# Optimization experiments

Hardware: AMD Instinct MI355X
Metric: run time of the kernel (lower is better)

## Reference

```python
import jax, jax.numpy as jnp
import numpy as np

EMBED_DIM = 1024
NUM_HEADS = 16
HEAD_DIM = EMBED_DIM // NUM_HEADS
ROPE_BASE = 10000.0


def _rope_angles(seq_len, head_dim):
    inv_freq = 1.0 / (ROPE_BASE ** (jnp.arange(0, head_dim, 2, dtype=jnp.float32) / head_dim))  # [D/2]
    pos = jnp.arange(seq_len, dtype=jnp.float32)
    ang = pos[:, None] * inv_freq[None, :]  # [S, D/2]
    return jnp.cos(ang), jnp.sin(ang)


def _apply_rope(t, cos, sin):
    # t: [B, H, S, D]; rotate-half convention
    d2 = t.shape[-1] // 2
    t1, t2 = t[..., :d2], t[..., d2:]
    return jnp.concatenate([t1 * cos - t2 * sin, t2 * cos + t1 * sin], axis=-1)


def setup_inputs() -> dict:
    key = jax.random.key(0)
    ks = jax.random.split(key, 6)
    B, S, E = 1, 4096, EMBED_DIM
    x = jax.random.normal(ks[0], (B, S, E), dtype=jnp.float32)
    # causal mask: True means masked-out (upper triangle above diagonal)
    mask = jnp.triu(jnp.ones((S, S), dtype=bool), k=1)[None, None, :, :]
    scale = 0.02
    wqkv_w = jax.random.normal(ks[1], (E, 3 * E), dtype=jnp.float32) * scale
    wqkv_b = jax.random.normal(ks[2], (3 * E,), dtype=jnp.float32) * scale
    out_w = jax.random.normal(ks[3], (E, E), dtype=jnp.float32) * scale
    out_b = jax.random.normal(ks[4], (E,), dtype=jnp.float32) * scale
    return {"x": x, "mask": mask, "wqkv_w": wqkv_w, "wqkv_b": wqkv_b, "out_w": out_w, "out_b": out_b}


def reference(x, mask, wqkv_w, wqkv_b, out_w, out_b):
    B, S, E = x.shape
    H, D = NUM_HEADS, HEAD_DIM
    qkv = x @ wqkv_w + wqkv_b  # [B, S, 3E]
    q, k, v = jnp.split(qkv, 3, axis=-1)
    # [B, S, E] -> [B, H, S, D]
    q = q.reshape(B, S, H, D).transpose(0, 2, 1, 3)
    k = k.reshape(B, S, H, D).transpose(0, 2, 1, 3)
    v = v.reshape(B, S, H, D).transpose(0, 2, 1, 3)
    cos, sin = _rope_angles(S, D)  # [S, D/2]
    q = _apply_rope(q, cos, sin)
    k = _apply_rope(k, cos, sin)
    scores = jnp.einsum('bhqd,bhkd->bhqk', q, k) * (D ** -0.5)  # [B, H, S, S]
    scores = jnp.where(mask[:, :, -S:, :], -jnp.inf, scores)
    weights = jax.nn.softmax(scores, axis=-1)
    ctx = jnp.einsum('bhqk,bhkd->bhqd', weights, v)  # [B, H, S, D]
    ctx = ctx.transpose(0, 2, 1, 3).reshape(B, S, E)
    return ctx @ out_w + out_b
```

## Files before the change

kernel.cpp:

```cpp
#include <hip/hip_runtime.h>
#include <hip/hip_bf16.h>
#include <math.h>

#define S_LEN 4096
#define EMB   1024
#define E3    3072
#define NH    16
#define HD    64

typedef unsigned short u16;
typedef short          bfrag __attribute__((ext_vector_type(8)));
typedef float          ffrag __attribute__((ext_vector_type(4)));
typedef unsigned short us8   __attribute__((ext_vector_type(8)));
typedef unsigned short us4   __attribute__((ext_vector_type(4)));

__device__ __forceinline__ u16 f2bf(float f) {
    union { float f; unsigned u; } v; v.f = f;
    unsigned r = v.u + 0x7fffu + ((v.u >> 16) & 1u);
    return (u16)(r >> 16);
}
__device__ __forceinline__ float bf2f(u16 b) {
    union { unsigned u; float f; } v; v.u = ((unsigned)b) << 16;
    return v.f;
}
__device__ __forceinline__ unsigned pack_bf16_trunc(float lo, float hi) {
    union { float f; unsigned u; } a, b; a.f = lo; b.f = hi;
    return __builtin_amdgcn_perm(b.u, a.u, 0x07060302u);
}
__device__ __forceinline__ void gld16(const void* g, void* l) {
    __builtin_amdgcn_global_load_lds(
        (const __attribute__((address_space(1))) unsigned int*)g,
        (__attribute__((address_space(3))) unsigned int*)l, 16, 0, 0);
}

__global__ __launch_bounds__(256)
void cast_bf16_kernel(const float* __restrict__ in, u16* __restrict__ out) {
    const size_t i = ((size_t)blockIdx.x * 256 + threadIdx.x) * 8;
    float4 a = *(const float4*)(in + i);
    float4 b = *(const float4*)(in + i + 4);
    us8 o;
    o[0]=f2bf(a.x); o[1]=f2bf(a.y); o[2]=f2bf(a.z); o[3]=f2bf(a.w);
    o[4]=f2bf(b.x); o[5]=f2bf(b.y); o[6]=f2bf(b.z); o[7]=f2bf(b.w);
    *(us8*)(out + i) = o;
}

__global__ __launch_bounds__(256)
void transpose_cast_kernel(const float* __restrict__ in, u16* __restrict__ out,
                           int R, int C) {
    __shared__ u16 T[64][72];
    const int r0 = blockIdx.x * 64, c0 = blockIdx.y * 64;
    const int t = threadIdx.x;
    const int rr = t >> 2, cc = (t & 3) * 16;

    const float* ip = in + (size_t)(r0 + rr) * C + c0 + cc;
    u16 tmp[16];
    #pragma unroll
    for (int i4 = 0; i4 < 4; i4++) {
        float4 v = ((const float4*)ip)[i4];
        tmp[4*i4+0]=f2bf(v.x); tmp[4*i4+1]=f2bf(v.y);
        tmp[4*i4+2]=f2bf(v.z); tmp[4*i4+3]=f2bf(v.w);
    }
    #pragma unroll
    for (int i8 = 0; i8 < 2; i8++) {
        us8 vv;
        #pragma unroll
        for (int j = 0; j < 8; j++) vv[j] = tmp[8*i8+j];
        *(us8*)&T[rr][cc + 8*i8] = vv;
    }
    __syncthreads();

    const int oc = t >> 2, orr = (t & 3) * 16;
    u16 ot[16];
    #pragma unroll
    for (int j = 0; j < 16; j++) ot[j] = T[orr + j][oc];
    u16* op = out + (size_t)(c0 + oc) * R + r0 + orr;
    #pragma unroll
    for (int i8 = 0; i8 < 2; i8++) {
        us8 vv;
        #pragma unroll
        for (int j = 0; j < 8; j++) vv[j] = ot[8*i8+j];
        *(us8*)(op + 8*i8) = vv;
    }
}

__global__ __launch_bounds__(256)
void transpose_v_kernel(const u16* __restrict__ qkvb, u16* __restrict__ vt) {
    __shared__ u16 T[64][72];
    const int s0 = blockIdx.x * 64, h = blockIdx.y;
    const int t = threadIdx.x;
    const int rr = t >> 2, cc = (t & 3) * 16;

    const u16* ip = qkvb + (size_t)(s0 + rr) * E3 + 2 * EMB + h * HD + cc;
    *(us8*)&T[rr][cc]     = *(const us8*)ip;
    *(us8*)&T[rr][cc + 8] = *(const us8*)(ip + 8);
    __syncthreads();

    const int od = t >> 2, os = (t & 3) * 16;
    u16 ot[16];
    #pragma unroll
    for (int j = 0; j < 16; j++) ot[j] = T[os + j][od];
    u16* op = vt + ((size_t)h * HD + od) * S_LEN + s0 + os;
    #pragma unroll
    for (int i8 = 0; i8 < 2; i8++) {
        us8 vv;
        #pragma unroll
        for (int j = 0; j < 8; j++) vv[j] = ot[8*i8+j];
        *(us8*)(op + 8*i8) = vv;
    }
}

__global__ __launch_bounds__(256)
void rope_bf16_kernel(u16* __restrict__ qkvb) {
    const int idx = blockIdx.x * blockDim.x + threadIdx.x;
    const int i = idx & 31;
    const int h = (idx >> 5) & (NH - 1);
    const int s = idx >> 9;

    const float inv_freq = exp2f(-(float)i * (13.287712379549449f / 32.0f));
    float sn, cs;
    sincosf((float)s * inv_freq, &sn, &cs);
    const float SC = 0.125f * 1.44269504088896f;

    size_t base = (size_t)s * E3 + h * HD;
    {
        float t1 = bf2f(qkvb[base + i]), t2 = bf2f(qkvb[base + i + 32]);
        qkvb[base + i]      = f2bf((t1 * cs - t2 * sn) * SC);
        qkvb[base + i + 32] = f2bf((t2 * cs + t1 * sn) * SC);
    }
    base += EMB;
    {
        float t1 = bf2f(qkvb[base + i]), t2 = bf2f(qkvb[base + i + 32]);
        qkvb[base + i]      = f2bf(t1 * cs - t2 * sn);
        qkvb[base + i + 32] = f2bf(t2 * cs + t1 * sn);
    }
}

template <int OUT_BF16>
__global__ __launch_bounds__(256, 2)
void gemm_bt_kernel(const u16* __restrict__ A, const u16* __restrict__ Bt,
                    const float* __restrict__ bias, void* __restrict__ Cv,
                    int M, int N, int K) {
    __shared__ u16 As[128][32];
    __shared__ u16 Bs[128][32];

    const int tid = threadIdx.x;
    const int w = tid >> 6, L = tid & 63;
    const int col = L & 15, quad = L >> 4;
    const int wm = w & 1, wn = w >> 1;
    const int m0 = blockIdx.x * 128, n0 = blockIdx.y * 128;

    ffrag acc[4][4];
    #pragma unroll
    for (int a = 0; a < 4; a++)
        #pragma unroll
        for (int b = 0; b < 4; b++)
            #pragma unroll
            for (int r = 0; r < 4; r++) acc[a][b][r] = 0.f;

    const int srow = L >> 2;
    const int schk = L & 3;

    for (int k0 = 0; k0 < K; k0 += 32) {
        __syncthreads();
        #pragma unroll
        for (int t = 0; t < 2; t++) {
            const int rg = (2 * w + t) * 16;
            gld16(A  + (size_t)(m0 + rg + srow) * K + k0 + schk * 8, &As[rg][0]);
            gld16(Bt + (size_t)(n0 + rg + srow) * K + k0 + schk * 8, &Bs[rg][0]);
        }
        __syncthreads();

        bfrag af[4], bf[4];
        #pragma unroll
        for (int mt = 0; mt < 4; mt++)
            af[mt] = *(const bfrag*)&As[64 * wm + 16 * mt + col][8 * quad];
        #pragma unroll
        for (int nt = 0; nt < 4; nt++)
            bf[nt] = *(const bfrag*)&Bs[64 * wn + 16 * nt + col][8 * quad];
        #pragma unroll
        for (int mt = 0; mt < 4; mt++)
            #pragma unroll
            for (int nt = 0; nt < 4; nt++)
                acc[mt][nt] = __builtin_amdgcn_mfma_f32_16x16x32_bf16(
                    af[mt], bf[nt], acc[mt][nt], 0, 0, 0);
    }

    float bv[4];
    #pragma unroll
    for (int nt = 0; nt < 4; nt++) bv[nt] = bias[n0 + 64 * wn + 16 * nt + col];

    #pragma unroll
    for (int mt = 0; mt < 4; mt++) {
        #pragma unroll
        for (int r = 0; r < 4; r++) {
            const int m = m0 + 64 * wm + 16 * mt + 4 * quad + r;
            #pragma unroll
            for (int nt = 0; nt < 4; nt++) {
                const int n = n0 + 64 * wn + 16 * nt + col;
                const float val = acc[mt][nt][r] + bv[nt];
                if (OUT_BF16) ((u16*)Cv)[(size_t)m * N + n] = f2bf(val);
                else          ((float*)Cv)[(size_t)m * N + n] = val;
            }
        }
    }
}

#define M0 16.0f

__global__ __launch_bounds__(256, 2)
void flash4_kernel(const u16* __restrict__ qkvb, const u16* __restrict__ vt,
                   u16* __restrict__ ctxb) {
    __shared__ u16 Qs[64][64];
    __shared__ u16 Ks[2][64][64];
    __shared__ u16 Vs[2][64][64];
    __shared__ u16 Ps[4][16][72];

    const int id = blockIdx.x;
    const int h = (id & 7) + ((id >> 8) << 3);
    const int p = (id >> 3) & 31;

    const int tid = threadIdx.x;
    const int w = tid >> 6, L = tid & 63;
    const int col = L & 15, quad = L >> 4;
    const int lr = L >> 3, lp = L & 7;
    const int lc = lp ^ lr;

    const size_t kArow = (size_t)(16 * w + lr) * E3 + EMB + h * HD + lc * 8;
    const size_t vArow = ((size_t)h * HD + 16 * w + lr) * S_LEN + lc * 8;

    #pragma unroll 1
    for (int phase = 0; phase < 2; phase++) {
        const int qi = phase ? (63 - p) : p;
        const int q0 = qi * 64;
        const int ntk = qi + 1;

        #pragma unroll
        for (int u = 0; u < 2; u++) {
            const int row = 16 * w + 8 * u;
            gld16(qkvb + (size_t)(q0 + row + lr) * E3 + h * HD + lc * 8,
                  &Qs[row][0]);
            gld16(qkvb + kArow + (size_t)(8 * u) * E3, &Ks[0][row][0]);
            gld16(vt + vArow + (size_t)(8 * u) * S_LEN, &Vs[0][row][0]);
        }
        __syncthreads();

        bfrag qf[2];
        #pragma unroll
        for (int ks = 0; ks < 2; ks++)
            qf[ks] = *(const bfrag*)
                &Qs[16 * w + col][(((4 * ks + quad) ^ (col & 7)) * 8)];

        ffrag o[4];
        #pragma unroll
        for (int d4 = 0; d4 < 4; d4++)
            #pragma unroll
            for (int r = 0; r < 4; r++) o[d4][r] = 0.f;
        float lsum = 0.f;

        #pragma unroll 1
        for (int t = 0; t < ntk; t++) {
            const int buf = t & 1;
            if (t + 1 < ntk) {
                const size_t ko = kArow + (size_t)(t + 1) * 64 * E3;
                const size_t vo = vArow + (size_t)(t + 1) * 64;
                #pragma unroll
                for (int u = 0; u < 2; u++) {
                    const int row = 16 * w + 8 * u;
                    gld16(qkvb + ko + (size_t)(8 * u) * E3, &Ks[buf ^ 1][row][0]);
                    gld16(vt + vo + (size_t)(8 * u) * S_LEN, &Vs[buf ^ 1][row][0]);
                }
            }

            ffrag st[4];
            #pragma unroll
            for (int t4 = 0; t4 < 4; t4++)
                #pragma unroll
                for (int r = 0; r < 4; r++) st[t4][r] = 0.f;
            #pragma unroll
            for (int ks = 0; ks < 2; ks++) {
                bfrag kf[4];
                #pragma unroll
                for (int t4 = 0; t4 < 4; t4++)
                    kf[t4] = *(const bfrag*)
                        &Ks[buf][16 * t4 + col][(((4 * ks + quad) ^ (col & 7)) * 8)];
                #pragma unroll
                for (int t4 = 0; t4 < 4; t4++)
                    st[t4] = __builtin_amdgcn_mfma_f32_16x16x32_bf16(
                        kf[t4], qf[ks], st[t4], 0, 0, 0);
            }

            if (t == ntk - 1) {
                const int qloc = 16 * w + col;
                #pragma unroll
                for (int t4 = 0; t4 < 4; t4++) {
                    const int key0 = 16 * t4 + 4 * quad;
                    #pragma unroll
                    for (int r = 0; r < 4; r++)
                        if (key0 + r > qloc) st[t4][r] = -3.0e38f;
                }
            }

            #pragma unroll
            for (int t4 = 0; t4 < 4; t4++) {
                float pr[4];
                #pragma unroll
                for (int r = 0; r < 4; r++) {
                    pr[r] = exp2f(st[t4][r] - M0);
                    lsum += pr[r];
                }
                uint2 pk;
                pk.x = pack_bf16_trunc(pr[0], pr[1]);
                pk.y = pack_bf16_trunc(pr[2], pr[3]);
                *(uint2*)&Ps[w][col][16 * t4 + 4 * quad] = pk;
            }

            #pragma unroll
            for (int ks = 0; ks < 2; ks++) {
                bfrag vf[4];
                #pragma unroll
                for (int d4 = 0; d4 < 4; d4++)
                    vf[d4] = *(const bfrag*)
                        &Vs[buf][16 * d4 + col][(((4 * ks + quad) ^ (col & 7)) * 8)];
                bfrag pf = *(const bfrag*)&Ps[w][col][32 * ks + 8 * quad];
                #pragma unroll
                for (int d4 = 0; d4 < 4; d4++)
                    o[d4] = __builtin_amdgcn_mfma_f32_16x16x32_bf16(
                        vf[d4], pf, o[d4], 0, 0, 0);
            }

            __syncthreads();
        }

        lsum += __shfl_xor(lsum, 16, 64);
        lsum += __shfl_xor(lsum, 32, 64);
        const float inv = 1.0f / lsum;
        const int qg = q0 + 16 * w + col;
        #pragma unroll
        for (int d4 = 0; d4 < 4; d4++) {
            us4 pk;
            #pragma unroll
            for (int r = 0; r < 4; r++) pk[r] = f2bf(o[d4][r] * inv);
            *(us4*)&ctxb[(size_t)qg * EMB + h * HD + 16 * d4 + 4 * quad] = pk;
        }
    }
}

extern "C" void kernel_launch(void* const* d_in, const int* in_sizes, int n_in,
                              void* d_out, int out_size, void* d_ws, size_t ws_size,
                              hipStream_t stream) {
    const float* x      = (const float*)d_in[0];
    const float* wqkv_w = (const float*)d_in[2];
    const float* wqkv_b = (const float*)d_in[3];
    const float* out_w  = (const float*)d_in[4];
    const float* out_b  = (const float*)d_in[5];
    float* out = (float*)d_out;

    u16* qkvb = (u16*)d_ws;
    u16* ctxb = qkvb + (size_t)S_LEN * E3;
    u16* xb   = ctxb + (size_t)S_LEN * EMB;
    u16* wt   = xb   + (size_t)S_LEN * EMB;
    u16* owt  = wt   + (size_t)E3 * EMB;
    u16* vtb  = owt  + (size_t)EMB * EMB;

    dim3 blk(256);

    cast_bf16_kernel<<<dim3(S_LEN * EMB / (256 * 8)), blk, 0, stream>>>(x, xb);
    transpose_cast_kernel<<<dim3(EMB / 64, E3 / 64), blk, 0, stream>>>(
        wqkv_w, wt, EMB, E3);
    transpose_cast_kernel<<<dim3(EMB / 64, EMB / 64), blk, 0, stream>>>(
        out_w, owt, EMB, EMB);

    gemm_bt_kernel<1><<<dim3(S_LEN / 128, E3 / 128), blk, 0, stream>>>(
        xb, wt, wqkv_b, qkvb, S_LEN, E3, EMB);

    rope_bf16_kernel<<<dim3(S_LEN * NH * 32 / 256), blk, 0, stream>>>(qkvb);
    transpose_v_kernel<<<dim3(S_LEN / 64, NH), blk, 0, stream>>>(qkvb, vtb);

    flash4_kernel<<<dim3(512), blk, 0, stream>>>(qkvb, vtb, ctxb);

    gemm_bt_kernel<0><<<dim3(S_LEN / 128, EMB / 128), blk, 0, stream>>>(
        ctxb, owt, out_b, out, S_LEN, EMB, EMB);
}
```

Before: 269.9 us.

## Double-buffer GEMM loads and split flash blocks per query tile with MFMA row sums

```diff
diff --git a/kernel.cpp b/kernel.cpp
--- a/kernel.cpp
+++ b/kernel.cpp
@@ -140,8 +140,8 @@
 void gemm_bt_kernel(const u16* __restrict__ A, const u16* __restrict__ Bt,
                     const float* __restrict__ bias, void* __restrict__ Cv,
                     int M, int N, int K) {
-    __shared__ u16 As[128][32];
-    __shared__ u16 Bs[128][32];
+    __shared__ u16 As[2][128][32];
+    __shared__ u16 Bs[2][128][32];
 
     const int tid = threadIdx.x;
     const int w = tid >> 6, L = tid & 63;
@@ -160,29 +160,42 @@
     const int srow = L >> 2;
     const int schk = L & 3;
 
-    for (int k0 = 0; k0 < K; k0 += 32) {
-        __syncthreads();
-        #pragma unroll
-        for (int t = 0; t < 2; t++) {
-            const int rg = (2 * w + t) * 16;
-            gld16(A  + (size_t)(m0 + rg + srow) * K + k0 + schk * 8, &As[rg][0]);
-            gld16(Bt + (size_t)(n0 + rg + srow) * K + k0 + schk * 8, &Bs[rg][0]);
-        }
-        __syncthreads();
+    #pragma unroll
+    for (int t = 0; t < 2; t++) {
+        const int rg = (2 * w + t) * 16;
+        gld16(A  + (size_t)(m0 + rg + srow) * K + schk * 8, &As[0][rg][0]);
+        gld16(Bt + (size_t)(n0 + rg + srow) * K + schk * 8, &Bs[0][rg][0]);
+    }
+    __syncthreads();
+
+    int buf = 0;
+    for (int k0 = 0; k0 < K; k0 += 32, buf ^= 1) {
+        if (k0 + 32 < K) {
+            #pragma unroll
+            for (int t = 0; t < 2; t++) {
+                const int rg = (2 * w + t) * 16;
+                gld16(A  + (size_t)(m0 + rg + srow) * K + k0 + 32 + schk * 8,
+                      &As[buf ^ 1][rg][0]);
+                gld16(Bt + (size_t)(n0 + rg + srow) * K + k0 + 32 + schk * 8,
+                      &Bs[buf ^ 1][rg][0]);
+            }
+        }
 
         bfrag af[4], bf[4];
         #pragma unroll
         for (int mt = 0; mt < 4; mt++)
-            af[mt] = *(const bfrag*)&As[64 * wm + 16 * mt + col][8 * quad];
+            af[mt] = *(const bfrag*)&As[buf][64 * wm + 16 * mt + col][8 * quad];
         #pragma unroll
         for (int nt = 0; nt < 4; nt++)
-            bf[nt] = *(const bfrag*)&Bs[64 * wn + 16 * nt + col][8 * quad];
+            bf[nt] = *(const bfrag*)&Bs[buf][64 * wn + 16 * nt + col][8 * quad];
         #pragma unroll
         for (int mt = 0; mt < 4; mt++)
             #pragma unroll
             for (int nt = 0; nt < 4; nt++)
                 acc[mt][nt] = __builtin_amdgcn_mfma_f32_16x16x32_bf16(
                     af[mt], bf[nt], acc[mt][nt], 0, 0, 0);
+
+        __syncthreads();
     }
 
     float bv[4];
@@ -205,19 +218,19 @@
     }
 }
 
-#define M0 16.0f
-
-__global__ __launch_bounds__(256, 2)
-void flash4_kernel(const u16* __restrict__ qkvb, const u16* __restrict__ vt,
+__global__ __launch_bounds__(256, 4)
+void flash5_kernel(const u16* __restrict__ qkvb, const u16* __restrict__ vt,
                    u16* __restrict__ ctxb) {
-    __shared__ u16 Qs[64][64];
+    __shared__ u16 QP[4][16][64];
     __shared__ u16 Ks[2][64][64];
     __shared__ u16 Vs[2][64][64];
-    __shared__ u16 Ps[4][16][72];
 
     const int id = blockIdx.x;
-    const int h = (id & 7) + ((id >> 8) << 3);
-    const int p = (id >> 3) & 31;
+    const int j  = (id >> 3) & 63;
+    const int h  = (id & 7) | ((id >> 9) << 3);
+    const int qi = (j < 32) ? j : 95 - j;
+    const int q0 = qi * 64;
+    const int ntk = qi + 1;
 
     const int tid = threadIdx.x;
     const int w = tid >> 6, L = tid & 63;
@@ -228,120 +241,114 @@
     const size_t kArow = (size_t)(16 * w + lr) * E3 + EMB + h * HD + lc * 8;
     const size_t vArow = ((size_t)h * HD + 16 * w + lr) * S_LEN + lc * 8;
 
+    #pragma unroll
+    for (int u = 0; u < 2; u++) {
+        gld16(qkvb + (size_t)(q0 + 16 * w + 8 * u + lr) * E3 + h * HD + lc * 8,
+              &QP[w][8 * u][0]);
+        gld16(qkvb + kArow + (size_t)(8 * u) * E3, &Ks[0][16 * w + 8 * u][0]);
+        gld16(vt + vArow + (size_t)(8 * u) * S_LEN, &Vs[0][16 * w + 8 * u][0]);
+    }
+    __syncthreads();
+
+    bfrag qf[2];
+    #pragma unroll
+    for (int ks = 0; ks < 2; ks++)
+        qf[ks] = *(const bfrag*)
+            ((const char*)&QP[w][col][0] + 16 * ((4 * ks + quad) ^ (col & 7)));
+
+    bfrag ones;
+    #pragma unroll
+    for (int i = 0; i < 8; i++) ones[i] = (short)0x3F80;
+
+    ffrag o[4], ol;
+    #pragma unroll
+    for (int d4 = 0; d4 < 4; d4++)
+        #pragma unroll
+        for (int r = 0; r < 4; r++) o[d4][r] = 0.f;
+    #pragma unroll
+    for (int r = 0; r < 4; r++) ol[r] = 0.f;
+
     #pragma unroll 1
-    for (int phase = 0; phase < 2; phase++) {
-        const int qi = phase ? (63 - p) : p;
-        const int q0 = qi * 64;
-        const int ntk = qi + 1;
-
-        #pragma unroll
-        for (int u = 0; u < 2; u++) {
-            const int row = 16 * w + 8 * u;
-            gld16(qkvb + (size_t)(q0 + row + lr) * E3 + h * HD + lc * 8,
-                  &Qs[row][0]);
-            gld16(qkvb + kArow + (size_t)(8 * u) * E3, &Ks[0][row][0]);
-            gld16(vt + vArow + (size_t)(8 * u) * S_LEN, &Vs[0][row][0]);
-        }
+    for (int t = 0; t < ntk; t++) {
+        const int buf = t & 1;
+        if (t + 1 < ntk) {
+            const size_t ko = kArow + (size_t)(t + 1) * 64 * E3;
+            const size_t vo = vArow + (size_t)(t + 1) * 64;
+            #pragma unroll
+            for (int u = 0; u < 2; u++) {
+                gld16(qkvb + ko + (size_t)(8 * u) * E3, &Ks[buf ^ 1][16 * w + 8 * u][0]);
+                gld16(vt + vo + (size_t)(8 * u) * S_LEN, &Vs[buf ^ 1][16 * w + 8 * u][0]);
+            }
+        }
+
+        ffrag st[4];
+        #pragma unroll
+        for (int t4 = 0; t4 < 4; t4++)
+            #pragma unroll
+            for (int r = 0; r < 4; r++) st[t4][r] = 0.f;
+        #pragma unroll
+        for (int ks = 0; ks < 2; ks++) {
+            bfrag kf[4];
+            #pragma unroll
+            for (int t4 = 0; t4 < 4; t4++)
+                kf[t4] = *(const bfrag*)
+                    &Ks[buf][16 * t4 + col][(((4 * ks + quad) ^ (col & 7)) * 8)];
+            #pragma unroll
+            for (int t4 = 0; t4 < 4; t4++)
+                st[t4] = __builtin_amdgcn_mfma_f32_16x16x32_bf16(
+                    kf[t4], qf[ks], st[t4], 0, 0, 0);
+        }
+
+        if (t == ntk - 1) {
+            const int qloc = 16 * w + col;
+            #pragma unroll
+            for (int t4 = 0; t4 < 4; t4++) {
+                const int key0 = 16 * t4 + 4 * quad;
+                #pragma unroll
+                for (int r = 0; r < 4; r++)
+                    if (key0 + r > qloc) st[t4][r] = -3.0e38f;
+            }
+        }
+
+        #pragma unroll
+        for (int t4 = 0; t4 < 4; t4++) {
+            float pr[4];
+            #pragma unroll
+            for (int r = 0; r < 4; r++) pr[r] = exp2f(st[t4][r]);
+            uint2 pk;
+            pk.x = pack_bf16_trunc(pr[0], pr[1]);
+            pk.y = pack_bf16_trunc(pr[2], pr[3]);
+            const int c2 = (2 * t4 + (quad >> 1)) ^ (col & 7);
+            *(uint2*)((char*)&QP[w][col][0] + 16 * c2 + 8 * (quad & 1)) = pk;
+        }
+
+        #pragma unroll
+        for (int ks = 0; ks < 2; ks++) {
+            bfrag vf[4];
+            #pragma unroll
+            for (int d4 = 0; d4 < 4; d4++)
+                vf[d4] = *(const bfrag*)
+                    &Vs[buf][16 * d4 + col][(((4 * ks + quad) ^ (col & 7)) * 8)];
+            bfrag pf = *(const bfrag*)
+                ((const char*)&QP[w][col][0] + 16 * ((4 * ks + quad) ^ (col & 7)));
+            #pragma unroll
+            for (int d4 = 0; d4 < 4; d4++)
+                o[d4] = __builtin_amdgcn_mfma_f32_16x16x32_bf16(
+                    vf[d4], pf, o[d4], 0, 0, 0);
+            ol = __builtin_amdgcn_mfma_f32_16x16x32_bf16(ones, pf, ol, 0, 0, 0);
+        }
+
         __syncthreads();
-
-        bfrag qf[2];
-        #pragma unroll
-        for (int ks = 0; ks < 2; ks++)
-            qf[ks] = *(const bfrag*)
-                &Qs[16 * w + col][(((4 * ks + quad) ^ (col & 7)) * 8)];
-
-        ffrag o[4];
-        #pragma unroll
-        for (int d4 = 0; d4 < 4; d4++)
-            #pragma unroll
-            for (int r = 0; r < 4; r++) o[d4][r] = 0.f;
-        float lsum = 0.f;
-
-        #pragma unroll 1
-        for (int t = 0; t < ntk; t++) {
-            const int buf = t & 1;
-            if (t + 1 < ntk) {
-                const size_t ko = kArow + (size_t)(t + 1) * 64 * E3;
-                const size_t vo = vArow + (size_t)(t + 1) * 64;
-                #pragma unroll
-                for (int u = 0; u < 2; u++) {
-                    const int row = 16 * w + 8 * u;
-                    gld16(qkvb + ko + (size_t)(8 * u) * E3, &Ks[buf ^ 1][row][0]);
-                    gld16(vt + vo + (size_t)(8 * u) * S_LEN, &Vs[buf ^ 1][row][0]);
-                }
-            }
-
-            ffrag st[4];
-            #pragma unroll
-            for (int t4 = 0; t4 < 4; t4++)
-                #pragma unroll
-                for (int r = 0; r < 4; r++) st[t4][r] = 0.f;
-            #pragma unroll
-            for (int ks = 0; ks < 2; ks++) {
-                bfrag kf[4];
-                #pragma unroll
-                for (int t4 = 0; t4 < 4; t4++)
-                    kf[t4] = *(const bfrag*)
-                        &Ks[buf][16 * t4 + col][(((4 * ks + quad) ^ (col & 7)) * 8)];
-                #pragma unroll
-                for (int t4 = 0; t4 < 4; t4++)
-                    st[t4] = __builtin_amdgcn_mfma_f32_16x16x32_bf16(
-                        kf[t4], qf[ks], st[t4], 0, 0, 0);
-            }
-
-            if (t == ntk - 1) {
-                const int qloc = 16 * w + col;
-                #pragma unroll
-                for (int t4 = 0; t4 < 4; t4++) {
-                    const int key0 = 16 * t4 + 4 * quad;
-                    #pragma unroll
-                    for (int r = 0; r < 4; r++)
-                        if (key0 + r > qloc) st[t4][r] = -3.0e38f;
-                }
-            }
-
-            #pragma unroll
-            for (int t4 = 0; t4 < 4; t4++) {
-                float pr[4];
-                #pragma unroll
-                for (int r = 0; r < 4; r++) {
-                    pr[r] = exp2f(st[t4][r] - M0);
-                    lsum += pr[r];
-                }
-                uint2 pk;
-                pk.x = pack_bf16_trunc(pr[0], pr[1]);
-                pk.y = pack_bf16_trunc(pr[2], pr[3]);
-                *(uint2*)&Ps[w][col][16 * t4 + 4 * quad] = pk;
-            }
-
-            #pragma unroll
-            for (int ks = 0; ks < 2; ks++) {
-                bfrag vf[4];
-                #pragma unroll
-                for (int d4 = 0; d4 < 4; d4++)
-                    vf[d4] = *(const bfrag*)
-                        &Vs[buf][16 * d4 + col][(((4 * ks + quad) ^ (col & 7)) * 8)];
-                bfrag pf = *(const bfrag*)&Ps[w][col][32 * ks + 8 * quad];
-                #pragma unroll
-                for (int d4 = 0; d4 < 4; d4++)
-                    o[d4] = __builtin_amdgcn_mfma_f32_16x16x32_bf16(
-                        vf[d4], pf, o[d4], 0, 0, 0);
-            }
-
-            __syncthreads();
-        }
-
-        lsum += __shfl_xor(lsum, 16, 64);
-        lsum += __shfl_xor(lsum, 32, 64);
-        const float inv = 1.0f / lsum;
-        const int qg = q0 + 16 * w + col;
-        #pragma unroll
-        for (int d4 = 0; d4 < 4; d4++) {
-            us4 pk;
-            #pragma unroll
-            for (int r = 0; r < 4; r++) pk[r] = f2bf(o[d4][r] * inv);
-            *(us4*)&ctxb[(size_t)qg * EMB + h * HD + 16 * d4 + 4 * quad] = pk;
-        }
+    }
+
+    const float inv = 1.0f / ol[0];
+    const int qg = q0 + 16 * w + col;
+    #pragma unroll
+    for (int d4 = 0; d4 < 4; d4++) {
+        us4 pk;
+        #pragma unroll
+        for (int r = 0; r < 4; r++) pk[r] = f2bf(o[d4][r] * inv);
+        *(us4*)&ctxb[(size_t)qg * EMB + h * HD + 16 * d4 + 4 * quad] = pk;
     }
 }
 
@@ -376,7 +383,7 @@
     rope_bf16_kernel<<<dim3(S_LEN * NH * 32 / 256), blk, 0, stream>>>(qkvb);
     transpose_v_kernel<<<dim3(S_LEN / 64, NH), blk, 0, stream>>>(qkvb, vtb);
 
-    flash4_kernel<<<dim3(512), blk, 0, stream>>>(qkvb, vtb, ctxb);
+    flash5_kernel<<<dim3(1024), blk, 0, stream>>>(qkvb, vtb, ctxb);
 
     gemm_bt_kernel<0><<<dim3(S_LEN / 128, EMB / 128), blk, 0, stream>>>(
         ctxb, owt, out_b, out, S_LEN, EMB, EMB);
```

Measured after the change: 267.4 us. About the same (-0.9%).
